# Kernel tuning notes

Measured on AMD Instinct MI355X. Metric: run time of the kernel, lower is better.

Reference implementation:

```python
import jax, jax.numpy as jnp
import numpy as np

N = 100000
E = 1600000
IN_CH = 128
OUT_CH = 512
NEG_SLOPE = 0.2
EPS = 1e-16


def _glorot(key, shape):
    fan_in, fan_out = shape[0], shape[-1]
    lim = float(np.sqrt(6.0 / (fan_in + fan_out)))
    return jax.random.uniform(key, shape, jnp.float32, -lim, lim)


def setup_inputs() -> dict:
    key = jax.random.key(0)
    ks = jax.random.split(key, 20)
    inp = {
        "x": jax.random.normal(ks[0], (N, IN_CH), jnp.float32),
        "edge_index": jax.random.randint(ks[1], (2, E), 0, N, jnp.int64),
        "edge_attr": jax.random.normal(ks[2], (E, 8), jnp.float32),
        # GATConv 1: 128 -> 32, heads=1, concat=True
        "W1": _glorot(ks[3], (IN_CH, 32)),
        "as1": _glorot(ks[4], (1, 32)),
        "ad1": _glorot(ks[5], (1, 32)),
        "b1": jnp.zeros((32,), jnp.float32),
        # GATConv 2: 32 -> 64, heads=1, concat=True
        "W2": _glorot(ks[6], (32, 64)),
        "as2": _glorot(ks[7], (1, 64)),
        "ad2": _glorot(ks[8], (1, 64)),
        "b2": jnp.zeros((64,), jnp.float32),
        # GATConv 3: 64 -> 64, heads=1, concat=False
        "W3": _glorot(ks[9], (64, 64)),
        "as3": _glorot(ks[10], (1, 64)),
        "ad3": _glorot(ks[11], (1, 64)),
        "b3": jnp.zeros((64,), jnp.float32),
        # Final Linear: 64 -> 512
        "Wl": _glorot(ks[12], (64, OUT_CH)),
        "bl": jnp.zeros((OUT_CH,), jnp.float32),
    }
    return inp


def _gat_layer(x, src, dst, W, a_src, a_dst, bias, heads, out_dim, concat):
    # Linear transform per head: [N, H, O]
    h = (x @ W).reshape(-1, heads, out_dim)
    # Per-node attention terms: [N, H]
    alpha_s = jnp.sum(h * a_src[None], axis=-1)
    alpha_d = jnp.sum(h * a_dst[None], axis=-1)
    # Edge logits with LeakyReLU: [E+N, H]
    e = jax.nn.leaky_relu(alpha_s[src] + alpha_d[dst], NEG_SLOPE)
    # Segment softmax over edges grouped by destination node
    m = jax.ops.segment_max(e, dst, num_segments=N)
    e = jnp.exp(e - m[dst])
    denom = jax.ops.segment_sum(e, dst, num_segments=N)
    alpha = e / (denom[dst] + EPS)  # [E+N, H]
    # Weighted message scatter-aggregate: [N, H, O]
    msg = h[src] * alpha[:, :, None]
    out = jax.ops.segment_sum(msg, dst, num_segments=N)
    if concat:
        out = out.reshape(-1, heads * out_dim)
    else:
        out = out.mean(axis=1)
    return out + bias


def reference(x, edge_index, edge_attr, W1, as1, ad1, b1, W2, as2, ad2, b2,
              W3, as3, ad3, b3, Wl, bl):
    # edge_dim=None -> edge_attr ignored by GATConv (lin_edge is None).
    # GATConv default add_self_loops=True: append (i, i) for every node.
    loops = jnp.arange(N, dtype=edge_index.dtype)
    src = jnp.concatenate([edge_index[0], loops])
    dst = jnp.concatenate([edge_index[1], loops])

    h = _gat_layer(x, src, dst, W1, as1, ad1, b1, heads=1, out_dim=32, concat=True)
    h = jax.nn.relu(h)
    h = _gat_layer(h, src, dst, W2, as2, ad2, b2, heads=1, out_dim=64, concat=True)
    h = jax.nn.relu(h)
    h = _gat_layer(h, src, dst, W3, as3, ad3, b3, heads=1, out_dim=64, concat=False)
    h = jax.nn.relu(h)
    return h @ Wl + bl
```

## Files before the change

kernel.cpp:

```cpp
#include <hip/hip_runtime.h>
#include <math.h>

namespace {

constexpr int NN = 100000;
constexpr int EE = 1600000;
constexpr float SLOPE = 0.2f;
constexpr float EPS_F = 1e-16f;
constexpr int NB = (NN + 255) / 256;

__device__ __forceinline__ float lrelu(float v) {
    return (v >= 0.f) ? v : SLOPE * v;
}

template <int IN, int OUT>
__global__ __launch_bounds__(256) void gemm_alpha(
    const float* __restrict__ x, const float* __restrict__ W,
    const float* __restrict__ avs, const float* __restrict__ avd,
    float* __restrict__ h, float* __restrict__ alps, float* __restrict__ alpd) {
    constexpr int TCg = OUT / 4;
    constexpr int TNg = 256 / TCg;
    constexpr int NODES = TNg * 4;
    constexpr int KC = (IN > 64) ? 64 : IN;
    constexpr int KCP = KC + 4;
    __shared__ __align__(16) float xl[NODES * KCP];
    const int tid = threadIdx.x;
    const int tc = tid % TCg;
    const int tn = tid / TCg;
    const int n0 = blockIdx.x * NODES;
    float acc[4][4] = {};

    for (int kc = 0; kc < IN; kc += KC) {
        __syncthreads();
        for (int i = tid * 4; i < NODES * KC; i += 1024) {
            int nl = i / KC, k = i % KC;
            int gn = n0 + nl;
            float4 v = make_float4(0.f, 0.f, 0.f, 0.f);
            if (gn < NN) v = *(const float4*)&x[(size_t)gn * IN + kc + k];
            *(float4*)&xl[nl * KCP + k] = v;
        }
        __syncthreads();
        for (int k = 0; k < KC; k += 4) {
            float4 hv[4];
#pragma unroll
            for (int j = 0; j < 4; ++j)
                hv[j] = *(const float4*)&xl[(j * TNg + tn) * KCP + k];
#pragma unroll
            for (int kk = 0; kk < 4; ++kk) {
                float4 wv = *(const float4*)&W[(size_t)(kc + k + kk) * OUT + tc * 4];
#pragma unroll
                for (int j = 0; j < 4; ++j) {
                    float hk = reinterpret_cast<const float*>(&hv[j])[kk];
                    acc[j][0] += hk * wv.x;
                    acc[j][1] += hk * wv.y;
                    acc[j][2] += hk * wv.z;
                    acc[j][3] += hk * wv.w;
                }
            }
        }
    }

    const float4 avsv = *(const float4*)&avs[tc * 4];
    const float4 avdv = *(const float4*)&avd[tc * 4];
#pragma unroll
    for (int j = 0; j < 4; ++j) {
        const int gn = n0 + j * TNg + tn;
        float4 o = make_float4(acc[j][0], acc[j][1], acc[j][2], acc[j][3]);
        if (gn < NN) *(float4*)&h[(size_t)gn * OUT + tc * 4] = o;
        float vs = o.x * avsv.x + o.y * avsv.y + o.z * avsv.z + o.w * avsv.w;
        float vd = o.x * avdv.x + o.y * avdv.y + o.z * avdv.z + o.w * avdv.w;
#pragma unroll
        for (int off = TCg / 2; off > 0; off >>= 1) {
            vs += __shfl_xor(vs, off, TCg);
            vd += __shfl_xor(vd, off, TCg);
        }
        if (tc == 0 && gn < NN) {
            alps[gn] = vs;
            alpd[gn] = vd;
        }
    }
}


__global__ __launch_bounds__(256) void deg_count(const int* __restrict__ ei,
                                                 int* __restrict__ deg) {
    int e = blockIdx.x * 256 + threadIdx.x;
    if (e < EE) atomicAdd(&deg[ei[EE + e]], 1);
}

__global__ __launch_bounds__(256) void scan_block(int* __restrict__ offs,
                                                  int* __restrict__ bsum) {
    __shared__ int tmp[256];
    const int t = threadIdx.x;
    const int i = blockIdx.x * 256 + t;
    int v = (i < NN) ? offs[i] : 0;
    tmp[t] = v;
    __syncthreads();
    int sum = v;
    for (int off = 1; off < 256; off <<= 1) {
        int add = (t >= off) ? tmp[t - off] : 0;
        __syncthreads();
        sum += add;
        tmp[t] = sum;
        __syncthreads();
    }
    if (i < NN) offs[i] = sum - v;
    if (t == 255) bsum[blockIdx.x] = sum;
}

__global__ __launch_bounds__(512) void scan_tops(int* __restrict__ bsum) {
    __shared__ int tmp[512];
    const int t = threadIdx.x;
    int v = (t < NB) ? bsum[t] : 0;
    tmp[t] = v;
    __syncthreads();
    int sum = v;
    for (int off = 1; off < 512; off <<= 1) {
        int add = (t >= off) ? tmp[t - off] : 0;
        __syncthreads();
        sum += add;
        tmp[t] = sum;
        __syncthreads();
    }
    if (t < NB) bsum[t] = sum - v;
}

__global__ __launch_bounds__(256) void scan_add(int* __restrict__ offs,
                                                const int* __restrict__ bsum,
                                                int* __restrict__ cursor) {
    const int i = blockIdx.x * 256 + threadIdx.x;
    if (i < NN) {
        int o = offs[i] + bsum[blockIdx.x];
        offs[i] = o;
        cursor[i] = o;
    }
}

__global__ __launch_bounds__(256) void csr_scatter(const int* __restrict__ ei,
                                                   int* __restrict__ cursor,
                                                   int* __restrict__ csr_src) {
    int e = blockIdx.x * 256 + threadIdx.x;
    if (e < EE) {
        int pos = atomicAdd(&cursor[ei[EE + e]], 1);
        csr_src[pos] = ei[e];
    }
}

template <int OUT>
__global__ __launch_bounds__(256) void gat_node_agg(
    const int* __restrict__ csr_src, const int* __restrict__ offs,
    const float* __restrict__ alps, const float* __restrict__ alpd,
    const float* __restrict__ h, const float* __restrict__ bias,
    float* __restrict__ out) {
    constexpr int L = OUT / 4;
    constexpr int NPB = 256 / L;
    const int tid = threadIdx.x;
    const int c4 = tid % L;
    const int n = blockIdx.x * NPB + tid / L;
    if (n >= NN) return;
    const int base = offs[n];
    const int end = (n + 1 < NN) ? offs[n + 1] : EE;
    const int dg = end - base;
    const float ad = alpd[n];

    const float p_self = __expf(fminf(lrelu(alps[n] + ad), 80.f));
    float denom = p_self;
    const float4 hs = *(const float4*)&h[(size_t)n * OUT + c4 * 4];
    float4 acc = make_float4(p_self * hs.x, p_self * hs.y, p_self * hs.z, p_self * hs.w);

    for (int j0 = 0; j0 < dg; j0 += L) {
        const int myj = j0 + c4;
        int s_c = 0;
        float p_c = 0.f;
        if (myj < dg) {
            s_c = csr_src[base + myj];
            p_c = __expf(fminf(lrelu(alps[s_c] + ad), 80.f));
        }
        float ps = p_c;
#pragma unroll
        for (int off = L / 2; off > 0; off >>= 1) ps += __shfl_xor(ps, off, L);
        denom += ps;
        const int lim = min(L, dg - j0);
        for (int j = 0; j < lim; ++j) {
            int s = __shfl(s_c, j, L);
            float p = __shfl(p_c, j, L);
            const float4 hv = *(const float4*)&h[(size_t)s * OUT + c4 * 4];
            acc.x += p * hv.x;
            acc.y += p * hv.y;
            acc.z += p * hv.z;
            acc.w += p * hv.w;
        }
    }
    const float inv = 1.f / (denom + EPS_F);
    const float4 bv = *(const float4*)&bias[c4 * 4];
    float4 o;
    o.x = fmaxf(acc.x * inv + bv.x, 0.f);
    o.y = fmaxf(acc.y * inv + bv.y, 0.f);
    o.z = fmaxf(acc.z * inv + bv.z, 0.f);
    o.w = fmaxf(acc.w * inv + bv.w, 0.f);
    *(float4*)&out[(size_t)n * OUT + c4 * 4] = o;
}

__global__ __launch_bounds__(256) void final_linear(
    const float* __restrict__ h, const float* __restrict__ W,
    const float* __restrict__ b, float* __restrict__ out) {
    __shared__ __align__(16) float hl[128 * 68];
    const int tid = threadIdx.x;
    const int tc = tid & 15;
    const int tn = tid >> 4;
    const int n0 = blockIdx.x * 128;

    for (int i = tid * 4; i < 128 * 64; i += 1024) {
        int nl = i >> 6, k = i & 63;
        int gn = n0 + nl;
        float4 v = make_float4(0.f, 0.f, 0.f, 0.f);
        if (gn < NN) v = *(const float4*)&h[(size_t)gn * 64 + k];
        *(float4*)&hl[nl * 68 + k] = v;
    }
    __syncthreads();

    for (int ct = 0; ct < 4; ++ct) {
        float acc[8][8] = {};
        for (int k = 0; k < 64; k += 4) {
            float4 hv[8];
#pragma unroll
            for (int j = 0; j < 8; ++j)
                hv[j] = *(const float4*)&hl[(j * 16 + tn) * 68 + k];
#pragma unroll
            for (int kk = 0; kk < 4; ++kk) {
                const float* wrow = &W[(size_t)(k + kk) * 512 + ct * 128 + tc * 8];
                float4 w0 = *(const float4*)wrow;
                float4 w1 = *(const float4*)(wrow + 4);
#pragma unroll
                for (int j = 0; j < 8; ++j) {
                    float hk = reinterpret_cast<const float*>(&hv[j])[kk];
                    acc[j][0] += hk * w0.x;
                    acc[j][1] += hk * w0.y;
                    acc[j][2] += hk * w0.z;
                    acc[j][3] += hk * w0.w;
                    acc[j][4] += hk * w1.x;
                    acc[j][5] += hk * w1.y;
                    acc[j][6] += hk * w1.z;
                    acc[j][7] += hk * w1.w;
                }
            }
        }
        const float* bp = &b[ct * 128 + tc * 8];
        const float4 b0 = *(const float4*)bp;
        const float4 b1 = *(const float4*)(bp + 4);
#pragma unroll
        for (int j = 0; j < 8; ++j) {
            int gn = n0 + j * 16 + tn;
            if (gn < NN) {
                float* op = &out[(size_t)gn * 512 + ct * 128 + tc * 8];
                float4 o0 = make_float4(acc[j][0] + b0.x, acc[j][1] + b0.y,
                                        acc[j][2] + b0.z, acc[j][3] + b0.w);
                float4 o1 = make_float4(acc[j][4] + b1.x, acc[j][5] + b1.y,
                                        acc[j][6] + b1.z, acc[j][7] + b1.w);
                *(float4*)op = o0;
                *(float4*)(op + 4) = o1;
            }
        }
    }
}

}

extern "C" void kernel_launch(void* const* d_in, const int* in_sizes, int n_in,
                              void* d_out, int out_size, void* d_ws, size_t ws_size,
                              hipStream_t stream) {
    const float* x = (const float*)d_in[0];
    const int* ei = (const int*)d_in[1];
    const float* W1 = (const float*)d_in[3];
    const float* as1 = (const float*)d_in[4];
    const float* ad1 = (const float*)d_in[5];
    const float* b1 = (const float*)d_in[6];
    const float* W2 = (const float*)d_in[7];
    const float* as2 = (const float*)d_in[8];
    const float* ad2 = (const float*)d_in[9];
    const float* b2 = (const float*)d_in[10];
    const float* W3 = (const float*)d_in[11];
    const float* as3 = (const float*)d_in[12];
    const float* ad3 = (const float*)d_in[13];
    const float* b3 = (const float*)d_in[14];
    const float* Wl = (const float*)d_in[15];
    const float* bl = (const float*)d_in[16];
    float* out = (float*)d_out;

    float* ws = (float*)d_ws;
    float* hbuf = ws;
    float* xbuf = hbuf + (size_t)NN * 64;
    float* asb = xbuf + (size_t)NN * 64;
    float* adb = asb + NN;
    int* offs = (int*)(adb + NN);
    int* cursor = offs + NN;
    int* bsum = cursor + NN;
    int* csr = bsum + 512;

    hipMemsetAsync(offs, 0, NN * sizeof(int), stream);
    deg_count<<<(EE + 255) / 256, 256, 0, stream>>>(ei, offs);
    scan_block<<<NB, 256, 0, stream>>>(offs, bsum);
    scan_tops<<<1, 512, 0, stream>>>(bsum);
    scan_add<<<NB, 256, 0, stream>>>(offs, bsum, cursor);
    csr_scatter<<<(EE + 255) / 256, 256, 0, stream>>>(ei, cursor, csr);

    gemm_alpha<128, 32><<<(NN + 127) / 128, 256, 0, stream>>>(x, W1, as1, ad1, hbuf, asb, adb);
    gat_node_agg<32><<<(NN + 31) / 32, 256, 0, stream>>>(csr, offs, asb, adb, hbuf, b1, xbuf);

    gemm_alpha<32, 64><<<(NN + 63) / 64, 256, 0, stream>>>(xbuf, W2, as2, ad2, hbuf, asb, adb);
    gat_node_agg<64><<<(NN + 15) / 16, 256, 0, stream>>>(csr, offs, asb, adb, hbuf, b2, xbuf);

    gemm_alpha<64, 64><<<(NN + 63) / 64, 256, 0, stream>>>(xbuf, W3, as3, ad3, hbuf, asb, adb);
    gat_node_agg<64><<<(NN + 15) / 16, 256, 0, stream>>>(csr, offs, asb, adb, hbuf, b3, xbuf);

    final_linear<<<(NN + 127) / 128, 256, 0, stream>>>(xbuf, Wl, bl, out);
}
```

Baseline: 863.0 us.

## Use one wavefront per node in GAT aggregation, retile final linear and gemm K-chunk

```diff
diff --git a/kernel.cpp b/kernel.cpp
--- a/kernel.cpp
+++ b/kernel.cpp
@@ -11,6 +11,10 @@
 
 __device__ __forceinline__ float lrelu(float v) {
     return (v >= 0.f) ? v : SLOPE * v;
+}
+
+__device__ __forceinline__ float readlane_f(float v, int l) {
+    return __uint_as_float(__builtin_amdgcn_readlane(__float_as_uint(v), l));
 }
 
 template <int IN, int OUT>
@@ -21,7 +25,7 @@
     constexpr int TCg = OUT / 4;
     constexpr int TNg = 256 / TCg;
     constexpr int NODES = TNg * 4;
-    constexpr int KC = (IN > 64) ? 64 : IN;
+    constexpr int KC = 32;
     constexpr int KCP = KC + 4;
     __shared__ __align__(16) float xl[NODES * KCP];
     const int tid = threadIdx.x;
@@ -147,17 +151,15 @@
 }
 
 template <int OUT>
-__global__ __launch_bounds__(256) void gat_node_agg(
+__global__ __launch_bounds__(256, 8) void gat_node_agg(
     const int* __restrict__ csr_src, const int* __restrict__ offs,
     const float* __restrict__ alps, const float* __restrict__ alpd,
     const float* __restrict__ h, const float* __restrict__ bias,
     float* __restrict__ out) {
-    constexpr int L = OUT / 4;
-    constexpr int NPB = 256 / L;
-    const int tid = threadIdx.x;
-    const int c4 = tid % L;
-    const int n = blockIdx.x * NPB + tid / L;
+    const int lane = threadIdx.x & 63;
+    const int n = blockIdx.x * 4 + (threadIdx.x >> 6);
     if (n >= NN) return;
+    const int c = lane & (OUT - 1);
     const int base = offs[n];
     const int end = (n + 1 < NN) ? offs[n + 1] : EE;
     const int dg = end - base;
@@ -165,52 +167,60 @@
 
     const float p_self = __expf(fminf(lrelu(alps[n] + ad), 80.f));
     float denom = p_self;
-    const float4 hs = *(const float4*)&h[(size_t)n * OUT + c4 * 4];
-    float4 acc = make_float4(p_self * hs.x, p_self * hs.y, p_self * hs.z, p_self * hs.w);
-
-    for (int j0 = 0; j0 < dg; j0 += L) {
-        const int myj = j0 + c4;
-        int s_c = 0;
-        float p_c = 0.f;
+    float acc = p_self * h[(size_t)n * OUT + c];
+
+    for (int j0 = 0; j0 < dg; j0 += 64) {
+        const int myj = j0 + lane;
+        int s_v = 0;
+        float p_v = 0.f;
         if (myj < dg) {
-            s_c = csr_src[base + myj];
-            p_c = __expf(fminf(lrelu(alps[s_c] + ad), 80.f));
-        }
-        float ps = p_c;
-#pragma unroll
-        for (int off = L / 2; off > 0; off >>= 1) ps += __shfl_xor(ps, off, L);
+            s_v = csr_src[base + myj];
+            p_v = __expf(fminf(lrelu(alps[s_v] + ad), 80.f));
+        }
+        float ps = p_v;
+#pragma unroll
+        for (int off = 32; off > 0; off >>= 1) ps += __shfl_xor(ps, off, 64);
         denom += ps;
-        const int lim = min(L, dg - j0);
-        for (int j = 0; j < lim; ++j) {
-            int s = __shfl(s_c, j, L);
-            float p = __shfl(p_c, j, L);
-            const float4 hv = *(const float4*)&h[(size_t)s * OUT + c4 * 4];
-            acc.x += p * hv.x;
-            acc.y += p * hv.y;
-            acc.z += p * hv.z;
-            acc.w += p * hv.w;
-        }
-    }
-    const float inv = 1.f / (denom + EPS_F);
-    const float4 bv = *(const float4*)&bias[c4 * 4];
-    float4 o;
-    o.x = fmaxf(acc.x * inv + bv.x, 0.f);
-    o.y = fmaxf(acc.y * inv + bv.y, 0.f);
-    o.z = fmaxf(acc.z * inv + bv.z, 0.f);
-    o.w = fmaxf(acc.w * inv + bv.w, 0.f);
-    *(float4*)&out[(size_t)n * OUT + c4 * 4] = o;
-}
-
-__global__ __launch_bounds__(256) void final_linear(
+        const int lim = min(64, dg - j0);
+        int j = 0;
+        for (; j + 3 < lim; j += 4) {
+            int s0 = __builtin_amdgcn_readlane(s_v, j);
+            int s1 = __builtin_amdgcn_readlane(s_v, j + 1);
+            int s2 = __builtin_amdgcn_readlane(s_v, j + 2);
+            int s3 = __builtin_amdgcn_readlane(s_v, j + 3);
+            float p0 = readlane_f(p_v, j);
+            float p1 = readlane_f(p_v, j + 1);
+            float p2 = readlane_f(p_v, j + 2);
+            float p3 = readlane_f(p_v, j + 3);
+            float h0 = h[(size_t)s0 * OUT + c];
+            float h1 = h[(size_t)s1 * OUT + c];
+            float h2 = h[(size_t)s2 * OUT + c];
+            float h3 = h[(size_t)s3 * OUT + c];
+            acc += p0 * h0;
+            acc += p1 * h1;
+            acc += p2 * h2;
+            acc += p3 * h3;
+        }
+        for (; j < lim; ++j) {
+            int s = __builtin_amdgcn_readlane(s_v, j);
+            float p = readlane_f(p_v, j);
+            acc += p * h[(size_t)s * OUT + c];
+        }
+    }
+    float v = acc / (denom + EPS_F) + bias[c];
+    if (lane < OUT) out[(size_t)n * OUT + c] = fmaxf(v, 0.f);
+}
+
+__global__ __launch_bounds__(256, 4) void final_linear(
     const float* __restrict__ h, const float* __restrict__ W,
     const float* __restrict__ b, float* __restrict__ out) {
-    __shared__ __align__(16) float hl[128 * 68];
+    __shared__ __align__(16) float hl[64 * 68];
     const int tid = threadIdx.x;
-    const int tc = tid & 15;
-    const int tn = tid >> 4;
-    const int n0 = blockIdx.x * 128;
-
-    for (int i = tid * 4; i < 128 * 64; i += 1024) {
+    const int tc = tid & 31;
+    const int tn = tid >> 5;
+    const int n0 = blockIdx.x * 64;
+
+    for (int i = tid * 4; i < 64 * 64; i += 1024) {
         int nl = i >> 6, k = i & 63;
         int gn = n0 + nl;
         float4 v = make_float4(0.f, 0.f, 0.f, 0.f);
@@ -219,16 +229,16 @@
     }
     __syncthreads();
 
-    for (int ct = 0; ct < 4; ++ct) {
+    for (int ct = 0; ct < 2; ++ct) {
         float acc[8][8] = {};
         for (int k = 0; k < 64; k += 4) {
             float4 hv[8];
 #pragma unroll
             for (int j = 0; j < 8; ++j)
-                hv[j] = *(const float4*)&hl[(j * 16 + tn) * 68 + k];
+                hv[j] = *(const float4*)&hl[(j * 8 + tn) * 68 + k];
 #pragma unroll
             for (int kk = 0; kk < 4; ++kk) {
-                const float* wrow = &W[(size_t)(k + kk) * 512 + ct * 128 + tc * 8];
+                const float* wrow = &W[(size_t)(k + kk) * 512 + ct * 256 + tc * 8];
                 float4 w0 = *(const float4*)wrow;
                 float4 w1 = *(const float4*)(wrow + 4);
 #pragma unroll
@@ -245,14 +255,14 @@
                 }
             }
         }
-        const float* bp = &b[ct * 128 + tc * 8];
+        const float* bp = &b[ct * 256 + tc * 8];
         const float4 b0 = *(const float4*)bp;
         const float4 b1 = *(const float4*)(bp + 4);
 #pragma unroll
         for (int j = 0; j < 8; ++j) {
-            int gn = n0 + j * 16 + tn;
+            int gn = n0 + j * 8 + tn;
             if (gn < NN) {
-                float* op = &out[(size_t)gn * 512 + ct * 128 + tc * 8];
+                float* op = &out[(size_t)gn * 512 + ct * 256 + tc * 8];
                 float4 o0 = make_float4(acc[j][0] + b0.x, acc[j][1] + b0.y,
                                         acc[j][2] + b0.z, acc[j][3] + b0.w);
                 float4 o1 = make_float4(acc[j][4] + b1.x, acc[j][5] + b1.y,
@@ -305,13 +315,13 @@
     csr_scatter<<<(EE + 255) / 256, 256, 0, stream>>>(ei, cursor, csr);
 
     gemm_alpha<128, 32><<<(NN + 127) / 128, 256, 0, stream>>>(x, W1, as1, ad1, hbuf, asb, adb);
-    gat_node_agg<32><<<(NN + 31) / 32, 256, 0, stream>>>(csr, offs, asb, adb, hbuf, b1, xbuf);
+    gat_node_agg<32><<<(NN + 3) / 4, 256, 0, stream>>>(csr, offs, asb, adb, hbuf, b1, xbuf);
 
     gemm_alpha<32, 64><<<(NN + 63) / 64, 256, 0, stream>>>(xbuf, W2, as2, ad2, hbuf, asb, adb);
-    gat_node_agg<64><<<(NN + 15) / 16, 256, 0, stream>>>(csr, offs, asb, adb, hbuf, b2, xbuf);
+    gat_node_agg<64><<<(NN + 3) / 4, 256, 0, stream>>>(csr, offs, asb, adb, hbuf, b2, xbuf);
 
     gemm_alpha<64, 64><<<(NN + 63) / 64, 256, 0, stream>>>(xbuf, W3, as3, ad3, hbuf, asb, adb);
-    gat_node_agg<64><<<(NN + 15) / 16, 256, 0, stream>>>(csr, offs, asb, adb, hbuf, b3, xbuf);
-
-    final_linear<<<(NN + 127) / 128, 256, 0, stream>>>(xbuf, Wl, bl, out);
-}
+    gat_node_agg<64><<<(NN + 3) / 4, 256, 0, stream>>>(csr, offs, asb, adb, hbuf, b3, xbuf);
+
+    final_linear<<<(NN + 63) / 64, 256, 0, stream>>>(xbuf, Wl, bl, out);
+}
```

Measured after the change: 893.4 us. 3.5% more time.
